# Kernel optimization log

Hardware: AMD Instinct MI355X
Metric: run time of the kernel (lower is better)

## Reference

```python
import jax, jax.numpy as jnp
import numpy as np

N_NODES = 100000
N_EDGES = 1600000
IN_DIM = 128
HID_DIM = 64


def setup_inputs() -> dict:
    key = jax.random.key(0)
    ks = jax.random.split(key, 8)
    feat = jax.random.normal(ks[0], (N_NODES, IN_DIM), dtype=jnp.float32)
    # xavier-normal-like scaling for gcn weights
    w1 = jax.random.normal(ks[1], (IN_DIM, HID_DIM), dtype=jnp.float32) * np.sqrt(2.0 / (IN_DIM + HID_DIM))
    w2 = jax.random.normal(ks[2], (HID_DIM, HID_DIM), dtype=jnp.float32) * np.sqrt(2.0 / (HID_DIM + HID_DIM))
    conv_w = jax.random.normal(ks[3], (2, 1, 3), dtype=jnp.float32) * np.sqrt(2.0 / 3.0)
    conv_b = jax.random.uniform(ks[4], (2,), dtype=jnp.float32, minval=-1.0 / np.sqrt(3.0), maxval=1.0 / np.sqrt(3.0))
    ref_radius = jnp.zeros((1,), dtype=jnp.float32)
    src = jax.random.randint(ks[5], (N_EDGES,), 0, N_NODES, dtype=jnp.int32)
    dst = jax.random.randint(ks[6], (N_EDGES,), 0, N_NODES, dtype=jnp.int32)
    return {"feat": feat, "w1": w1, "w2": w2, "conv_w": conv_w, "conv_b": conv_b,
            "ref_radius": ref_radius, "src": src, "dst": dst}


def _dropout(h, key, p=0.5):
    keep = jax.random.bernoulli(key, 1.0 - p, h.shape)
    return jnp.where(keep, h / (1.0 - p), 0.0)


def _gcn(h, w, norm, src2, dst2, n, pre_matmul):
    # norm-scale -> (matmul) -> copy_src/sum scatter -> (matmul) -> norm-scale -> relu
    h = h * norm[:, None]
    if pre_matmul:  # in_feats > out_feats branch
        h = h @ w
        agg = jax.ops.segment_sum(h[src2], dst2, num_segments=n)
    else:
        agg = jax.ops.segment_sum(h[src2], dst2, num_segments=n)
        agg = agg @ w
    rst = agg * norm[:, None]
    return jax.nn.relu(rst)


def reference(feat, w1, w2, conv_w, conv_b, ref_radius, src, dst):
    n = feat.shape[0]
    # dgl.add_self_loop
    loops = jnp.arange(n, dtype=src.dtype)
    src2 = jnp.concatenate([src, loops])
    dst2 = jnp.concatenate([dst, loops])
    deg = jax.ops.segment_sum(jnp.ones_like(dst2, dtype=jnp.float32), dst2, num_segments=n)
    norm = jnp.clip(deg, 1.0, None) ** -0.5  # [n]

    dkey = jax.random.key(42)
    k1, k2 = jax.random.split(dkey)

    h = _gcn(feat, w1, norm, src2, dst2, n, pre_matmul=True)   # 128 > 64
    h = _dropout(h, k1)
    h = _gcn(h, w2, norm, src2, dst2, n, pre_matmul=False)     # 64 == 64
    h = _dropout(h, k2)

    # conv1d: [n, hid] -> [n, 1, hid] -> [n, 2, hid-2] -> [n, 2*(hid-2)]
    x = h[:, None, :]
    y = jax.lax.conv_general_dilated(x, conv_w, window_strides=(1,), padding='VALID',
                                     dimension_numbers=('NCH', 'OIH', 'NCH'))
    y = y + conv_b[None, :, None]
    h = y.reshape(n, -1)

    # hypersphere: distance of each node feature from the centroid vs ref radius
    o = jnp.mean(h, axis=0)
    radius = jnp.sqrt(jnp.sum((h - o + 1e-6) ** 2, axis=1))  # F.pairwise_distance eps=1e-6
    dis = jnp.clip(radius - ref_radius, 1e-4, 1.0 - 1e-4)
    return dis, ref_radius
```

## Files before the change

### kernel.cpp

```cpp
#include <hip/hip_runtime.h>
#include <stdint.h>

#define HID 64
#define INDIM 128
#define NBK 512
#define NBLK 512
#define EPBCAP 3200
#define BK3CAP 8192
#define CSREP 32

typedef __attribute__((ext_vector_type(8))) short bf16x8;
typedef __attribute__((ext_vector_type(4))) float f32x4;
typedef __attribute__((ext_vector_type(2))) float f32x2;

__host__ __device__ __forceinline__ void tf2x32(uint32_t k0, uint32_t k1,
                                                uint32_t x0, uint32_t x1,
                                                uint32_t& o0, uint32_t& o1) {
  uint32_t ks2 = k0 ^ k1 ^ 0x1BD11BDAu;
#define ROTL(v, r) (((v) << (r)) | ((v) >> (32 - (r))))
#define RND(r) { x0 += x1; x1 = ROTL(x1, r); x1 ^= x0; }
  x0 += k0; x1 += k1;
  RND(13) RND(15) RND(26) RND(6)
  x0 += k1; x1 += ks2 + 1u;
  RND(17) RND(29) RND(16) RND(24)
  x0 += ks2; x1 += k0 + 2u;
  RND(13) RND(15) RND(26) RND(6)
  x0 += k0; x1 += k1 + 3u;
  RND(17) RND(29) RND(16) RND(24)
  x0 += k1; x1 += ks2 + 4u;
  RND(13) RND(15) RND(26) RND(6)
  x0 += ks2; x1 += k0 + 5u;
  o0 = x0; o1 = x1;
#undef RND
#undef ROTL
}

__device__ __forceinline__ float tf_uniform(uint32_t ka, uint32_t kb, uint32_t j) {
  uint32_t o0, o1;
  tf2x32(ka, kb, 0u, j, o0, o1);
  uint32_t bits = o0 ^ o1;
  uint32_t f = (bits >> 9) | 0x3f800000u;
  return __uint_as_float(f) - 1.0f;
}

__device__ __forceinline__ unsigned short f2bf(float f) {
  uint32_t x = __float_as_uint(f);
  uint32_t r = (x + 0x7fffu + ((x >> 16) & 1u)) >> 16;
  return (unsigned short)r;
}

__device__ __forceinline__ float bf2f_lo(uint32_t u) { return __uint_as_float(u << 16); }
__device__ __forceinline__ float bf2f_hi(uint32_t u) { return __uint_as_float(u & 0xffff0000u); }

__device__ __forceinline__ unsigned char f2fp8(float v) {
  return (unsigned char)(__builtin_amdgcn_cvt_pk_fp8_f32(v, 0.f, 0, false) & 0xff);
}

__global__ __launch_bounds__(256) void binsort_k(const int* __restrict__ src,
                                                 const int* __restrict__ dst,
                                                 uint32_t* __restrict__ sorted,
                                                 int* __restrict__ blockoff2,
                                                 const float* __restrict__ w1,
                                                 const float* __restrict__ w2,
                                                 unsigned short* __restrict__ w1t,
                                                 unsigned short* __restrict__ w2t,
                                                 float* __restrict__ colsumR,
                                                 int E, int EPB, int NB) {
  __shared__ uint32_t lbuf[EPBCAP];
  __shared__ int dbuf[EPBCAP];
  __shared__ int ha[NBK], hb[NBK], cursor[NBK];
  int b = blockIdx.x, t = threadIdx.x;
  {
    int i = b * 256 + t;
    if (i < CSREP * HID) colsumR[i] = 0.f;
    if (i < INDIM * HID) {
      int c = i >> 7, k = i & 127;
      w1t[i] = f2bf(w1[k * HID + c]);
    } else if (i < INDIM * HID + HID * HID) {
      int j = i - INDIM * HID;
      int c = j >> 6, k = j & 63;
      w2t[j] = f2bf(w2[k * HID + c]);
    }
  }
  int e0 = b * EPB;
  int e1 = e0 + EPB; if (e1 > E) e1 = E;
  int m = e1 - e0;
  ha[t] = 0; ha[t + 256] = 0;
  __syncthreads();
  for (int i = t; i < m; i += 256) {
    int d = dst[e0 + i];
    dbuf[i] = d;
    atomicAdd(&ha[d >> 8], 1);
  }
  __syncthreads();
  int* cur = ha; int* nxt = hb;
  for (int off = 1; off < 512; off <<= 1) {
    int i0 = t, i1 = t + 256;
    int v0 = cur[i0] + ((i0 >= off) ? cur[i0 - off] : 0);
    int v1 = cur[i1] + ((i1 >= off) ? cur[i1 - off] : 0);
    __syncthreads();
    nxt[i0] = v0; nxt[i1] = v1;
    __syncthreads();
    int* tmp = cur; cur = nxt; nxt = tmp;
  }
  for (int i = t; i < NB; i += 256) {
    int ex = (i == 0) ? 0 : cur[i - 1];
    cursor[i] = ex;
    blockoff2[(size_t)i * NBLK + b] = ex;
  }
  if (t == 0) blockoff2[(size_t)NB * NBLK + b] = m;
  __syncthreads();
  for (int i = t; i < m; i += 256) {
    int d = dbuf[i], s = src[e0 + i];
    int pos = atomicAdd(&cursor[d >> 8], 1);
    lbuf[pos] = ((uint32_t)s << 8) | (uint32_t)(d & 255);
  }
  __syncthreads();
  for (int i = t; i < m; i += 256) sorted[e0 + i] = lbuf[i];
}

__global__ __launch_bounds__(256) void csrbuild_k(const uint32_t* __restrict__ sorted,
                                                  const int* __restrict__ blockoff2,
                                                  int* __restrict__ rowstart,
                                                  int* __restrict__ csr,
                                                  float* __restrict__ norm,
                                                  int NB, int n, int E, int EPB) {
  __shared__ uint32_t ebuf[BK3CAP];
  __shared__ int sa[256], sb[256], cursor[256];
  __shared__ int sc_[NBLK], sd_[NBLK];
  int bid = blockIdx.x, t = threadIdx.x;
  int xcd = bid & 7, sub = bid >> 3;
  int qq = NB >> 3, rr = NB & 7;
  int k = (xcd < rr ? xcd * (qq + 1) : rr * (qq + 1) + (xcd - rr) * qq) + sub;

  int b0 = t, b1 = t + 256;
  int lo0 = blockoff2[(size_t)k * NBLK + b0];
  int lo1 = blockoff2[(size_t)k * NBLK + b1];
  int hi0 = blockoff2[(size_t)(k + 1) * NBLK + b0];
  int hi1 = blockoff2[(size_t)(k + 1) * NBLK + b1];
  int len0 = hi0 - lo0, len1 = hi1 - lo1;
  sa[t] = lo0 + lo1;
  sc_[b0] = len0; sc_[b1] = len1;
  __syncthreads();
  for (int off = 128; off > 0; off >>= 1) {
    if (t < off) sa[t] += sa[t + off];
    __syncthreads();
  }
  int s0 = sa[0];
  int* cur = sc_; int* nxt = sd_;
  for (int off = 1; off < NBLK; off <<= 1) {
    int v0 = cur[b0] + ((b0 >= off) ? cur[b0 - off] : 0);
    int v1 = cur[b1] + ((b1 >= off) ? cur[b1 - off] : 0);
    __syncthreads();
    nxt[b0] = v0; nxt[b1] = v1;
    __syncthreads();
    int* tmp = cur; cur = nxt; nxt = tmp;
  }
  int M = cur[NBLK - 1];
  int dd0 = cur[b0] - len0, dd1 = cur[b1] - len1;
  {
    const uint32_t* sp = sorted + (size_t)b0 * EPB;
    for (int i = lo0; i < hi0; i++) ebuf[dd0 + (i - lo0)] = sp[i];
  }
  {
    const uint32_t* sp = sorted + (size_t)b1 * EPB;
    for (int i = lo1; i < hi1; i++) ebuf[dd1 + (i - lo1)] = sp[i];
  }
  cursor[t] = 0;
  __syncthreads();
  for (int i = t; i < M; i += 256) atomicAdd(&cursor[ebuf[i] & 255], 1);
  __syncthreads();
  int cnt = cursor[t];
  sa[t] = cnt;
  int* cu2 = sa; int* nx2 = sb;
  __syncthreads();
  for (int off = 1; off < 256; off <<= 1) {
    int v = cu2[t] + ((t >= off) ? cu2[t - off] : 0);
    __syncthreads();
    nx2[t] = v;
    __syncthreads();
    int* tmp = cu2; cu2 = nx2; nx2 = tmp;
  }
  int localrow = cu2[t] - cnt;
  int node = k * 256 + t;
  if (node < n) {
    rowstart[node] = s0 + localrow;
    norm[node] = rsqrtf((float)(cnt + 1));
  }
  if (k == NB - 1 && t == 255) rowstart[n] = E;
  cursor[t] = localrow;
  __syncthreads();
  for (int i = t; i < M; i += 256) {
    uint32_t pe = ebuf[i];
    int pos = atomicAdd(&cursor[pe & 255], 1);
    csr[s0 + pos] = (int)(pe >> 8);
  }
}

__global__ __launch_bounds__(256) void gemm1(const float* __restrict__ feat,
                                             const unsigned short* __restrict__ w1t,
                                             const float* __restrict__ norm,
                                             unsigned char* __restrict__ h0, int n) {
  int t = threadIdx.x;
  int wv = t >> 6, lane = t & 63;
  int strip = blockIdx.x * 4 + wv;
  if (strip * 16 >= n) return;
  int m = lane & 15, q = lane >> 4;
  bf16x8 Bf[4][4];
#pragma unroll
  for (int kc = 0; kc < 4; kc++)
#pragma unroll
    for (int ct = 0; ct < 4; ct++)
      Bf[kc][ct] = *(const bf16x8*)(w1t + (ct * 16 + m) * INDIM + kc * 32 + q * 8);
  const float* arow = feat + (size_t)(strip * 16 + m) * INDIM;
  bf16x8 Af[4];
#pragma unroll
  for (int kc = 0; kc < 4; kc++) {
    const float* pa = arow + kc * 32 + q * 8;
    bf16x8 a;
#pragma unroll
    for (int j = 0; j < 8; j++) a[j] = (short)f2bf(pa[j]);
    Af[kc] = a;
  }
  f32x4 acc[4] = {{0.f,0.f,0.f,0.f},{0.f,0.f,0.f,0.f},{0.f,0.f,0.f,0.f},{0.f,0.f,0.f,0.f}};
#pragma unroll
  for (int kc = 0; kc < 4; kc++)
#pragma unroll
    for (int ct = 0; ct < 4; ct++)
      acc[ct] = __builtin_amdgcn_mfma_f32_16x16x32_bf16(Af[kc], Bf[kc][ct], acc[ct], 0, 0, 0);
#pragma unroll
  for (int r = 0; r < 4; r++) {
    int row = strip * 16 + q * 4 + r;
    float nm = norm[row];
#pragma unroll
    for (int ct = 0; ct < 4; ct++)
      h0[(size_t)row * HID + ct * 16 + m] = f2fp8(acc[ct][r] * nm);
  }
}

template <int MODE>
__global__ __launch_bounds__(256) void gather_k(const uint32_t* __restrict__ h8,
                                                void* __restrict__ outp,
                                                const int* __restrict__ rowstart,
                                                const int* __restrict__ csr,
                                                const float* __restrict__ norm,
                                                int n, uint32_t ka, uint32_t kb) {
  int wid = (int)((blockIdx.x * 256u + threadIdx.x) >> 6);
  int d0 = wid * 4;
  if (d0 >= n) return;
  int lane = threadIdx.x & 63;
  int g = lane >> 4, c4 = lane & 15;
  int g4 = g << 2;

  int rr = d0 + (lane < 4 ? lane : 4);
  if (rr > n) rr = n;
  int rsl = rowstart[rr];
  int r0[5];
#pragma unroll
  for (int i = 0; i < 5; ++i) r0[i] = __shfl(rsl, i);
  int L[4];
#pragma unroll
  for (int i = 0; i < 4; ++i) L[i] = r0[i + 1] - r0[i];

  int selfrow = d0 + g; if (selfrow >= n) selfrow = d0;
  uint32_t uself = h8[(size_t)selfrow * 16 + c4];

  int idx[4];
#pragma unroll
  for (int i = 0; i < 4; ++i) {
    int la = L[i] < 32 ? L[i] : 32;
    idx[i] = (lane < la) ? csr[r0[i] + lane] : 0;
  }

  uint32_t u[4][8];
#pragma unroll
  for (int i = 0; i < 4; ++i) {
#pragma unroll
    for (int t = 0; t < 8; ++t) {
      int s = __builtin_amdgcn_ds_bpermute(16 * t + g4, idx[i]);
      u[i][t] = (4 * t + g < L[i]) ? h8[(size_t)(uint32_t)s * 16 + c4] : 0u;
    }
  }

  f32x2 al[4], ah[4];
#pragma unroll
  for (int i = 0; i < 4; ++i) { al[i] = (f32x2){0.f, 0.f}; ah[i] = (f32x2){0.f, 0.f}; }
#pragma unroll
  for (int i = 0; i < 4; ++i) {
#pragma unroll
    for (int t = 0; t < 8; ++t) {
      al[i] += __builtin_amdgcn_cvt_pk_f32_fp8((int)u[i][t], false);
      ah[i] += __builtin_amdgcn_cvt_pk_f32_fp8((int)u[i][t], true);
    }
  }

#pragma unroll
  for (int i = 0; i < 4; ++i) {
    if (L[i] > 32) {
      for (int e0 = 32; e0 < L[i]; e0 += 4) {
        int e = e0 + g;
        uint32_t uu = 0u;
        if (e < L[i]) {
          int s = csr[r0[i] + e];
          uu = h8[(size_t)(uint32_t)s * 16 + c4];
        }
        al[i] += __builtin_amdgcn_cvt_pk_f32_fp8((int)uu, false);
        ah[i] += __builtin_amdgcn_cvt_pk_f32_fp8((int)uu, true);
      }
    }
  }

  f32x2 sl, sh, rl2, rh2;
  sl = (g & 1) ? al[0] : al[1];
  sh = (g & 1) ? ah[0] : ah[1];
  rl2.x = __shfl_xor(sl.x, 16); rl2.y = __shfl_xor(sl.y, 16);
  rh2.x = __shfl_xor(sh.x, 16); rh2.y = __shfl_xor(sh.y, 16);
  f32x2 fABl = ((g & 1) ? al[1] : al[0]) + rl2;
  f32x2 fABh = ((g & 1) ? ah[1] : ah[0]) + rh2;
  sl = (g & 1) ? al[2] : al[3];
  sh = (g & 1) ? ah[2] : ah[3];
  rl2.x = __shfl_xor(sl.x, 16); rl2.y = __shfl_xor(sl.y, 16);
  rh2.x = __shfl_xor(sh.x, 16); rh2.y = __shfl_xor(sh.y, 16);
  f32x2 fCDl = ((g & 1) ? al[3] : al[2]) + rl2;
  f32x2 fCDh = ((g & 1) ? ah[3] : ah[2]) + rh2;
  sl = (g & 2) ? fABl : fCDl;
  sh = (g & 2) ? fABh : fCDh;
  rl2.x = __shfl_xor(sl.x, 32); rl2.y = __shfl_xor(sl.y, 32);
  rh2.x = __shfl_xor(sh.x, 32); rh2.y = __shfl_xor(sh.y, 32);
  f32x2 tl = ((g & 2) ? fCDl : fABl) + rl2;
  f32x2 th = ((g & 2) ? fCDh : fABh) + rh2;

  tl += __builtin_amdgcn_cvt_pk_f32_fp8((int)uself, false);
  th += __builtin_amdgcn_cvt_pk_f32_fp8((int)uself, true);

  int d = d0 + g;
  float a0 = tl.x, a1 = tl.y, a2 = th.x, a3 = th.y;
  if (MODE == 0) {
    uint32_t jb = (uint32_t)d0 * 64u + (uint32_t)lane;
    float u0 = tf_uniform(ka, kb, jb);
    float u1 = tf_uniform(ka, kb, jb + 64u);
    float u2 = tf_uniform(ka, kb, jb + 128u);
    float u3 = tf_uniform(ka, kb, jb + 192u);
    unsigned long long kp0 = __ballot(u0 < 0.5f);
    unsigned long long kp1 = __ballot(u1 < 0.5f);
    unsigned long long kp2 = __ballot(u2 < 0.5f);
    unsigned long long kp3 = __ballot(u3 < 0.5f);
    unsigned long long keep = (g & 2) ? ((g & 1) ? kp3 : kp2)
                                      : ((g & 1) ? kp1 : kp0);
    uint32_t kb4 = (uint32_t)(keep >> (4 * c4)) & 15u;
    float nm = norm[d < n ? d : d0];
    float v0 = fmaxf(a0 * nm, 0.f), v1 = fmaxf(a1 * nm, 0.f);
    float v2 = fmaxf(a2 * nm, 0.f), v3 = fmaxf(a3 * nm, 0.f);
    float s2 = 2.f * nm;
    v0 = (kb4 & 1u) ? v0 * s2 : 0.f;
    v1 = (kb4 & 2u) ? v1 * s2 : 0.f;
    v2 = (kb4 & 4u) ? v2 * s2 : 0.f;
    v3 = (kb4 & 8u) ? v3 * s2 : 0.f;
    if (d < n) {
      int o = __builtin_amdgcn_cvt_pk_fp8_f32(v0, v1, 0, false);
      o = __builtin_amdgcn_cvt_pk_fp8_f32(v2, v3, o, true);
      ((uint32_t*)outp)[(size_t)d * 16 + c4] = (uint32_t)o;
    }
  } else {
    if (d < n) {
      uint2 w;
      w.x = (uint32_t)f2bf(a0) | ((uint32_t)f2bf(a1) << 16);
      w.y = (uint32_t)f2bf(a2) | ((uint32_t)f2bf(a3) << 16);
      ((uint2*)outp)[(size_t)d * 16 + c4] = w;
    }
  }
}

__global__ __launch_bounds__(256) void gemm2(const unsigned short* __restrict__ aggbf,
                                             const unsigned short* __restrict__ w2t,
                                             const float* __restrict__ norm,
                                             unsigned short* __restrict__ h2,
                                             float* __restrict__ colsumR, int n,
                                             uint32_t ka, uint32_t kb) {
  __shared__ float red[4][HID];
  int t = threadIdx.x;
  int wv = t >> 6, lane = t & 63;
  int strip = blockIdx.x * 4 + wv;
  int m = lane & 15, q = lane >> 4;
  float cs[4] = {0.f, 0.f, 0.f, 0.f};
  bool active = (strip * 16 < n);
  if (active) {
    bf16x8 Bf[2][4];
#pragma unroll
    for (int kc = 0; kc < 2; kc++)
#pragma unroll
      for (int ct = 0; ct < 4; ct++)
        Bf[kc][ct] = *(const bf16x8*)(w2t + (ct * 16 + m) * HID + kc * 32 + q * 8);
    const unsigned short* arow = aggbf + (size_t)(strip * 16 + m) * HID;
    bf16x8 Af[2];
#pragma unroll
    for (int kc = 0; kc < 2; kc++)
      Af[kc] = *(const bf16x8*)(arow + kc * 32 + q * 8);
    f32x4 acc[4] = {{0.f,0.f,0.f,0.f},{0.f,0.f,0.f,0.f},{0.f,0.f,0.f,0.f},{0.f,0.f,0.f,0.f}};
#pragma unroll
    for (int kc = 0; kc < 2; kc++)
#pragma unroll
      for (int ct = 0; ct < 4; ct++)
        acc[ct] = __builtin_amdgcn_mfma_f32_16x16x32_bf16(Af[kc], Bf[kc][ct], acc[ct], 0, 0, 0);
#pragma unroll
    for (int r = 0; r < 4; r++) {
      int row = strip * 16 + q * 4 + r;
      float nm = norm[row];
#pragma unroll
      for (int ct = 0; ct < 4; ct++) {
        int col = ct * 16 + m;
        float v = fmaxf(acc[ct][r] * nm, 0.f);
        float u = tf_uniform(ka, kb, (uint32_t)row * 64u + (uint32_t)col);
        v = (u < 0.5f) ? v * 2.f : 0.f;
        h2[(size_t)row * HID + col] = f2bf(v);
        cs[ct] += v;
      }
    }
  }
#pragma unroll
  for (int ct = 0; ct < 4; ct++) {
    cs[ct] += __shfl_xor(cs[ct], 16);
    cs[ct] += __shfl_xor(cs[ct], 32);
  }
  if (q == 0) {
    red[wv][m] = cs[0];
    red[wv][16 + m] = cs[1];
    red[wv][32 + m] = cs[2];
    red[wv][48 + m] = cs[3];
  }
  __syncthreads();
  if (t < HID) {
    float v = red[0][t] + red[1][t] + red[2][t] + red[3][t];
    atomicAdd(&colsumR[(blockIdx.x & (CSREP - 1)) * HID + t], v);
  }
}

__global__ __launch_bounds__(128) void final_k(const uint32_t* __restrict__ h2u,
                                               const float* __restrict__ colsumR,
                                               const float* __restrict__ conv_w,
                                               const float* __restrict__ conv_b,
                                               const float* __restrict__ ref_radius,
                                               float* __restrict__ out, int n) {
  __shared__ float rows[128 * 67];
  __shared__ float omean[124];
  __shared__ float cm[HID];
  int t = threadIdx.x;
  int node0 = blockIdx.x * 128;
  if (t < HID) {
    float s = 0.f;
#pragma unroll
    for (int r = 0; r < CSREP; r++) s += colsumR[r * HID + t];
    cm[t] = s * (1.0f / (float)n);
  }
  for (int idx = t; idx < 128 * 32; idx += 128) {
    int r = idx >> 5, cpi = idx & 31;
    int node = node0 + r;
    uint32_t u = (node < n) ? h2u[(size_t)node * 32 + cpi] : 0u;
    rows[r * 67 + 2 * cpi] = bf2f_lo(u);
    rows[r * 67 + 2 * cpi + 1] = bf2f_hi(u);
  }
  __syncthreads();
  if (t < 124) {
    int o = t / 62, i = t % 62;
    omean[t] = conv_b[o] + conv_w[o * 3] * cm[i] + conv_w[o * 3 + 1] * cm[i + 1] +
               conv_w[o * 3 + 2] * cm[i + 2];
  }
  __syncthreads();
  int node = node0 + t;
  if (node < n) {
    float r0[HID];
#pragma unroll
    for (int k = 0; k < HID; k++) r0[k] = rows[t * 67 + k];
    float w00 = conv_w[0], w01 = conv_w[1], w02 = conv_w[2];
    float w10 = conv_w[3], w11 = conv_w[4], w12 = conv_w[5];
    float b0 = conv_b[0], b1 = conv_b[1];
    float acc = 0.f;
#pragma unroll
    for (int i = 0; i < 62; i++) {
      float y0 = b0 + w00 * r0[i] + w01 * r0[i + 1] + w02 * r0[i + 2];
      float d0 = y0 - omean[i] + 1e-6f;
      acc += d0 * d0;
      float y1 = b1 + w10 * r0[i] + w11 * r0[i + 1] + w12 * r0[i + 2];
      float d1 = y1 - omean[62 + i] + 1e-6f;
      acc += d1 * d1;
    }
    float radius = sqrtf(acc);
    float dis = fminf(fmaxf(radius - ref_radius[0], 1e-4f), 1.f - 1e-4f);
    out[node] = dis;
  }
  if (blockIdx.x == 0 && t == 0) out[n] = ref_radius[0];
}

extern "C" void kernel_launch(void* const* d_in, const int* in_sizes, int n_in,
                              void* d_out, int out_size, void* d_ws, size_t ws_size,
                              hipStream_t stream) {
  const float* feat = (const float*)d_in[0];
  const float* w1 = (const float*)d_in[1];
  const float* w2 = (const float*)d_in[2];
  const float* conv_w = (const float*)d_in[3];
  const float* conv_b = (const float*)d_in[4];
  const float* ref_radius = (const float*)d_in[5];
  const int* src = (const int*)d_in[6];
  const int* dst = (const int*)d_in[7];
  int n = in_sizes[0] / INDIM;
  int E = in_sizes[6];
  float* out = (float*)d_out;

  int NB = (n + 255) >> 8;
  int EPB = (E + NBLK - 1) / NBLK;

  char* p = (char*)d_ws;
  auto carve = [&](size_t bytes) { void* r = (void*)p; p += (bytes + 255) & ~(size_t)255; return r; };
  float* norm = (float*)carve((size_t)n * 4);
  float* colsumR = (float*)carve((size_t)CSREP * HID * 4);
  int* rowstart = (int*)carve(((size_t)n + 1) * 4);
  int* blockoff2 = (int*)carve((size_t)(NB + 1) * NBLK * 4);
  uint32_t* sorted = (uint32_t*)carve((size_t)E * 4);
  int* csr = (int*)carve((size_t)E * 4);
  unsigned short* w1t = (unsigned short*)carve((size_t)INDIM * HID * 2);
  unsigned short* w2t = (unsigned short*)carve((size_t)HID * HID * 2);
  unsigned char* H0f8 = (unsigned char*)carve((size_t)n * HID);
  unsigned char* Tf8 = (unsigned char*)carve((size_t)n * HID);
  unsigned short* Abf = (unsigned short*)carve((size_t)n * HID * 2);
  unsigned short* H2bf = (unsigned short*)carve((size_t)n * HID * 2);

  uint32_t k1a, k1b, k2a, k2b;
  tf2x32(0u, 42u, 0u, 0u, k1a, k1b);
  tf2x32(0u, 42u, 0u, 1u, k2a, k2b);

  int gatherB = (n + 15) / 16;
  int stripB = ((n + 15) / 16 + 3) / 4;

  binsort_k<<<NBLK, 256, 0, stream>>>(src, dst, sorted, blockoff2, w1, w2, w1t, w2t, colsumR, E, EPB, NB);
  csrbuild_k<<<NB, 256, 0, stream>>>(sorted, blockoff2, rowstart, csr, norm, NB, n, E, EPB);
  gemm1<<<stripB, 256, 0, stream>>>(feat, w1t, norm, H0f8, n);
  gather_k<0><<<gatherB, 256, 0, stream>>>((const uint32_t*)H0f8, Tf8, rowstart, csr, norm, n, k1a, k1b);
  gather_k<1><<<gatherB, 256, 0, stream>>>((const uint32_t*)Tf8, Abf, rowstart, csr, norm, n, 0u, 0u);
  gemm2<<<stripB, 256, 0, stream>>>(Abf, w2t, norm, H2bf, colsumR, n, k2a, k2b);
  final_k<<<(n + 127) / 128, 128, 0, stream>>>((const uint32_t*)H2bf, colsumR, conv_w, conv_b, ref_radius, out, n);
}
```

Before: 233.8 us.

## Fuse second-layer gather with gemm2 through shared memory tile

After: 233.3 us. No clear change (-0.2%).

```diff
diff --git a/kernel.cpp b/kernel.cpp
--- a/kernel.cpp
+++ b/kernel.cpp
@@ -238,9 +238,8 @@
   }
 }
 
-template <int MODE>
 __global__ __launch_bounds__(256) void gather_k(const uint32_t* __restrict__ h8,
-                                                void* __restrict__ outp,
+                                                uint32_t* __restrict__ outp,
                                                 const int* __restrict__ rowstart,
                                                 const int* __restrict__ csr,
                                                 const float* __restrict__ norm,
@@ -334,84 +333,165 @@
   th += __builtin_amdgcn_cvt_pk_f32_fp8((int)uself, true);
 
   int d = d0 + g;
-  float a0 = tl.x, a1 = tl.y, a2 = th.x, a3 = th.y;
-  if (MODE == 0) {
-    uint32_t jb = (uint32_t)d0 * 64u + (uint32_t)lane;
-    float u0 = tf_uniform(ka, kb, jb);
-    float u1 = tf_uniform(ka, kb, jb + 64u);
-    float u2 = tf_uniform(ka, kb, jb + 128u);
-    float u3 = tf_uniform(ka, kb, jb + 192u);
-    unsigned long long kp0 = __ballot(u0 < 0.5f);
-    unsigned long long kp1 = __ballot(u1 < 0.5f);
-    unsigned long long kp2 = __ballot(u2 < 0.5f);
-    unsigned long long kp3 = __ballot(u3 < 0.5f);
-    unsigned long long keep = (g & 2) ? ((g & 1) ? kp3 : kp2)
-                                      : ((g & 1) ? kp1 : kp0);
-    uint32_t kb4 = (uint32_t)(keep >> (4 * c4)) & 15u;
-    float nm = norm[d < n ? d : d0];
-    float v0 = fmaxf(a0 * nm, 0.f), v1 = fmaxf(a1 * nm, 0.f);
-    float v2 = fmaxf(a2 * nm, 0.f), v3 = fmaxf(a3 * nm, 0.f);
-    float s2 = 2.f * nm;
-    v0 = (kb4 & 1u) ? v0 * s2 : 0.f;
-    v1 = (kb4 & 2u) ? v1 * s2 : 0.f;
-    v2 = (kb4 & 4u) ? v2 * s2 : 0.f;
-    v3 = (kb4 & 8u) ? v3 * s2 : 0.f;
-    if (d < n) {
-      int o = __builtin_amdgcn_cvt_pk_fp8_f32(v0, v1, 0, false);
-      o = __builtin_amdgcn_cvt_pk_fp8_f32(v2, v3, o, true);
-      ((uint32_t*)outp)[(size_t)d * 16 + c4] = (uint32_t)o;
-    }
-  } else {
-    if (d < n) {
-      uint2 w;
-      w.x = (uint32_t)f2bf(a0) | ((uint32_t)f2bf(a1) << 16);
-      w.y = (uint32_t)f2bf(a2) | ((uint32_t)f2bf(a3) << 16);
-      ((uint2*)outp)[(size_t)d * 16 + c4] = w;
-    }
-  }
-}
-
-__global__ __launch_bounds__(256) void gemm2(const unsigned short* __restrict__ aggbf,
-                                             const unsigned short* __restrict__ w2t,
-                                             const float* __restrict__ norm,
-                                             unsigned short* __restrict__ h2,
-                                             float* __restrict__ colsumR, int n,
-                                             uint32_t ka, uint32_t kb) {
-  __shared__ float red[4][HID];
+  uint32_t jb = (uint32_t)d0 * 64u + (uint32_t)lane;
+  float u0 = tf_uniform(ka, kb, jb);
+  float u1 = tf_uniform(ka, kb, jb + 64u);
+  float u2 = tf_uniform(ka, kb, jb + 128u);
+  float u3 = tf_uniform(ka, kb, jb + 192u);
+  unsigned long long kp0 = __ballot(u0 < 0.5f);
+  unsigned long long kp1 = __ballot(u1 < 0.5f);
+  unsigned long long kp2 = __ballot(u2 < 0.5f);
+  unsigned long long kp3 = __ballot(u3 < 0.5f);
+  unsigned long long keep = (g & 2) ? ((g & 1) ? kp3 : kp2)
+                                    : ((g & 1) ? kp1 : kp0);
+  uint32_t kb4 = (uint32_t)(keep >> (4 * c4)) & 15u;
+  float nm = norm[d < n ? d : d0];
+  float v0 = fmaxf(tl.x * nm, 0.f), v1 = fmaxf(tl.y * nm, 0.f);
+  float v2 = fmaxf(th.x * nm, 0.f), v3 = fmaxf(th.y * nm, 0.f);
+  float s2 = 2.f * nm;
+  v0 = (kb4 & 1u) ? v0 * s2 : 0.f;
+  v1 = (kb4 & 2u) ? v1 * s2 : 0.f;
+  v2 = (kb4 & 4u) ? v2 * s2 : 0.f;
+  v3 = (kb4 & 8u) ? v3 * s2 : 0.f;
+  if (d < n) {
+    int o = __builtin_amdgcn_cvt_pk_fp8_f32(v0, v1, 0, false);
+    o = __builtin_amdgcn_cvt_pk_fp8_f32(v2, v3, o, true);
+    outp[(size_t)d * 16 + c4] = (uint32_t)o;
+  }
+}
+
+__global__ __launch_bounds__(256) void gather2gemm2_k(
+    const uint32_t* __restrict__ h8, const int* __restrict__ rowstart,
+    const int* __restrict__ csr, const float* __restrict__ norm,
+    const unsigned short* __restrict__ w2t, unsigned short* __restrict__ h2,
+    float* __restrict__ colsumR, int n, uint32_t ka, uint32_t kb) {
+  __shared__ unsigned short abuf[16][72];
   int t = threadIdx.x;
   int wv = t >> 6, lane = t & 63;
-  int strip = blockIdx.x * 4 + wv;
+  int node0 = blockIdx.x * 16;
+  int d0 = node0 + wv * 4;
+  int g = lane >> 4, c4 = lane & 15;
+  int g4 = g << 2;
+  int lrow = (wv << 2) + g;
+
+  if (d0 < n) {
+    int rr = d0 + (lane < 4 ? lane : 4);
+    if (rr > n) rr = n;
+    int rsl = rowstart[rr];
+    int r0[5];
+#pragma unroll
+    for (int i = 0; i < 5; ++i) r0[i] = __shfl(rsl, i);
+    int L[4];
+#pragma unroll
+    for (int i = 0; i < 4; ++i) L[i] = r0[i + 1] - r0[i];
+
+    int selfrow = d0 + g; if (selfrow >= n) selfrow = d0;
+    uint32_t uself = h8[(size_t)selfrow * 16 + c4];
+
+    int idx[4];
+#pragma unroll
+    for (int i = 0; i < 4; ++i) {
+      int la = L[i] < 32 ? L[i] : 32;
+      idx[i] = (lane < la) ? csr[r0[i] + lane] : 0;
+    }
+
+    uint32_t u[4][8];
+#pragma unroll
+    for (int i = 0; i < 4; ++i) {
+#pragma unroll
+      for (int tt = 0; tt < 8; ++tt) {
+        int s = __builtin_amdgcn_ds_bpermute(16 * tt + g4, idx[i]);
+        u[i][tt] = (4 * tt + g < L[i]) ? h8[(size_t)(uint32_t)s * 16 + c4] : 0u;
+      }
+    }
+
+    f32x2 al[4], ah[4];
+#pragma unroll
+    for (int i = 0; i < 4; ++i) { al[i] = (f32x2){0.f, 0.f}; ah[i] = (f32x2){0.f, 0.f}; }
+#pragma unroll
+    for (int i = 0; i < 4; ++i) {
+#pragma unroll
+      for (int tt = 0; tt < 8; ++tt) {
+        al[i] += __builtin_amdgcn_cvt_pk_f32_fp8((int)u[i][tt], false);
+        ah[i] += __builtin_amdgcn_cvt_pk_f32_fp8((int)u[i][tt], true);
+      }
+    }
+
+#pragma unroll
+    for (int i = 0; i < 4; ++i) {
+      if (L[i] > 32) {
+        for (int e0 = 32; e0 < L[i]; e0 += 4) {
+          int e = e0 + g;
+          uint32_t uu = 0u;
+          if (e < L[i]) {
+            int s = csr[r0[i] + e];
+            uu = h8[(size_t)(uint32_t)s * 16 + c4];
+          }
+          al[i] += __builtin_amdgcn_cvt_pk_f32_fp8((int)uu, false);
+          ah[i] += __builtin_amdgcn_cvt_pk_f32_fp8((int)uu, true);
+        }
+      }
+    }
+
+    f32x2 sl, sh, rl2, rh2;
+    sl = (g & 1) ? al[0] : al[1];
+    sh = (g & 1) ? ah[0] : ah[1];
+    rl2.x = __shfl_xor(sl.x, 16); rl2.y = __shfl_xor(sl.y, 16);
+    rh2.x = __shfl_xor(sh.x, 16); rh2.y = __shfl_xor(sh.y, 16);
+    f32x2 fABl = ((g & 1) ? al[1] : al[0]) + rl2;
+    f32x2 fABh = ((g & 1) ? ah[1] : ah[0]) + rh2;
+    sl = (g & 1) ? al[2] : al[3];
+    sh = (g & 1) ? ah[2] : ah[3];
+    rl2.x = __shfl_xor(sl.x, 16); rl2.y = __shfl_xor(sl.y, 16);
+    rh2.x = __shfl_xor(sh.x, 16); rh2.y = __shfl_xor(sh.y, 16);
+    f32x2 fCDl = ((g & 1) ? al[3] : al[2]) + rl2;
+    f32x2 fCDh = ((g & 1) ? ah[3] : ah[2]) + rh2;
+    sl = (g & 2) ? fABl : fCDl;
+    sh = (g & 2) ? fABh : fCDh;
+    rl2.x = __shfl_xor(sl.x, 32); rl2.y = __shfl_xor(sl.y, 32);
+    rh2.x = __shfl_xor(sh.x, 32); rh2.y = __shfl_xor(sh.y, 32);
+    f32x2 tl = ((g & 2) ? fCDl : fABl) + rl2;
+    f32x2 th = ((g & 2) ? fCDh : fABh) + rh2;
+
+    tl += __builtin_amdgcn_cvt_pk_f32_fp8((int)uself, false);
+    th += __builtin_amdgcn_cvt_pk_f32_fp8((int)uself, true);
+
+    uint2 w;
+    w.x = (uint32_t)f2bf(tl.x) | ((uint32_t)f2bf(tl.y) << 16);
+    w.y = (uint32_t)f2bf(th.x) | ((uint32_t)f2bf(th.y) << 16);
+    if (d0 + g >= n) { w.x = 0u; w.y = 0u; }
+    *(uint2*)&abuf[lrow][4 * c4] = w;
+  } else {
+    uint2 z; z.x = 0u; z.y = 0u;
+    *(uint2*)&abuf[lrow][4 * c4] = z;
+  }
+  __syncthreads();
+  if (wv != 0) return;
+  if (node0 >= n) return;
+
   int m = lane & 15, q = lane >> 4;
+  f32x4 acc[4] = {{0.f,0.f,0.f,0.f},{0.f,0.f,0.f,0.f},{0.f,0.f,0.f,0.f},{0.f,0.f,0.f,0.f}};
+#pragma unroll
+  for (int kc = 0; kc < 2; kc++) {
+    bf16x8 Af = *(const bf16x8*)&abuf[m][kc * 32 + q * 8];
+#pragma unroll
+    for (int ct = 0; ct < 4; ct++) {
+      bf16x8 Bf = *(const bf16x8*)(w2t + (ct * 16 + m) * HID + kc * 32 + q * 8);
+      acc[ct] = __builtin_amdgcn_mfma_f32_16x16x32_bf16(Af, Bf, acc[ct], 0, 0, 0);
+    }
+  }
   float cs[4] = {0.f, 0.f, 0.f, 0.f};
-  bool active = (strip * 16 < n);
-  if (active) {
-    bf16x8 Bf[2][4];
-#pragma unroll
-    for (int kc = 0; kc < 2; kc++)
-#pragma unroll
-      for (int ct = 0; ct < 4; ct++)
-        Bf[kc][ct] = *(const bf16x8*)(w2t + (ct * 16 + m) * HID + kc * 32 + q * 8);
-    const unsigned short* arow = aggbf + (size_t)(strip * 16 + m) * HID;
-    bf16x8 Af[2];
-#pragma unroll
-    for (int kc = 0; kc < 2; kc++)
-      Af[kc] = *(const bf16x8*)(arow + kc * 32 + q * 8);
-    f32x4 acc[4] = {{0.f,0.f,0.f,0.f},{0.f,0.f,0.f,0.f},{0.f,0.f,0.f,0.f},{0.f,0.f,0.f,0.f}};
-#pragma unroll
-    for (int kc = 0; kc < 2; kc++)
-#pragma unroll
-      for (int ct = 0; ct < 4; ct++)
-        acc[ct] = __builtin_amdgcn_mfma_f32_16x16x32_bf16(Af[kc], Bf[kc][ct], acc[ct], 0, 0, 0);
-#pragma unroll
-    for (int r = 0; r < 4; r++) {
-      int row = strip * 16 + q * 4 + r;
+#pragma unroll
+  for (int r = 0; r < 4; r++) {
+    int row = node0 + q * 4 + r;
+    if (row < n) {
       float nm = norm[row];
 #pragma unroll
       for (int ct = 0; ct < 4; ct++) {
         int col = ct * 16 + m;
         float v = fmaxf(acc[ct][r] * nm, 0.f);
-        float u = tf_uniform(ka, kb, (uint32_t)row * 64u + (uint32_t)col);
-        v = (u < 0.5f) ? v * 2.f : 0.f;
+        float uu = tf_uniform(ka, kb, (uint32_t)row * 64u + (uint32_t)col);
+        v = (uu < 0.5f) ? v * 2.f : 0.f;
         h2[(size_t)row * HID + col] = f2bf(v);
         cs[ct] += v;
       }
@@ -423,15 +503,9 @@
     cs[ct] += __shfl_xor(cs[ct], 32);
   }
   if (q == 0) {
-    red[wv][m] = cs[0];
-    red[wv][16 + m] = cs[1];
-    red[wv][32 + m] = cs[2];
-    red[wv][48 + m] = cs[3];
-  }
-  __syncthreads();
-  if (t < HID) {
-    float v = red[0][t] + red[1][t] + red[2][t] + red[3][t];
-    atomicAdd(&colsumR[(blockIdx.x & (CSREP - 1)) * HID + t], v);
+    float* dstc = colsumR + (blockIdx.x & (CSREP - 1)) * HID;
+#pragma unroll
+    for (int ct = 0; ct < 4; ct++) atomicAdd(&dstc[ct * 16 + m], cs[ct]);
   }
 }
 
@@ -521,7 +595,6 @@
   unsigned short* w2t = (unsigned short*)carve((size_t)HID * HID * 2);
   unsigned char* H0f8 = (unsigned char*)carve((size_t)n * HID);
   unsigned char* Tf8 = (unsigned char*)carve((size_t)n * HID);
-  unsigned short* Abf = (unsigned short*)carve((size_t)n * HID * 2);
   unsigned short* H2bf = (unsigned short*)carve((size_t)n * HID * 2);
 
   uint32_t k1a, k1b, k2a, k2b;
@@ -534,8 +607,7 @@
   binsort_k<<<NBLK, 256, 0, stream>>>(src, dst, sorted, blockoff2, w1, w2, w1t, w2t, colsumR, E, EPB, NB);
   csrbuild_k<<<NB, 256, 0, stream>>>(sorted, blockoff2, rowstart, csr, norm, NB, n, E, EPB);
   gemm1<<<stripB, 256, 0, stream>>>(feat, w1t, norm, H0f8, n);
-  gather_k<0><<<gatherB, 256, 0, stream>>>((const uint32_t*)H0f8, Tf8, rowstart, csr, norm, n, k1a, k1b);
-  gather_k<1><<<gatherB, 256, 0, stream>>>((const uint32_t*)Tf8, Abf, rowstart, csr, norm, n, 0u, 0u);
-  gemm2<<<stripB, 256, 0, stream>>>(Abf, w2t, norm, H2bf, colsumR, n, k2a, k2b);
+  gather_k<<<gatherB, 256, 0, stream>>>((const uint32_t*)H0f8, (uint32_t*)Tf8, rowstart, csr, norm, n, k1a, k1b);
+  gather2gemm2_k<<<gatherB, 256, 0, stream>>>((const uint32_t*)Tf8, rowstart, csr, norm, w2t, H2bf, colsumR, n, k2a, k2b);
   final_k<<<(n + 127) / 128, 128, 0, stream>>>((const uint32_t*)H2bf, colsumR, conv_w, conv_b, ref_radius, out, n);
 }
```
